# Kernel optimization log

Hardware: AMD Instinct MI355X
Metric: run time of the kernel (lower is better)

## Reference

```python
import jax, jax.numpy as jnp
import numpy as np

WINDOWS = [2, 4, 6]
THR = 0.5


def conv1x1(x, w, b):
    # x: [N,C,H,W], w: [O,C], b: [O]
    return jnp.einsum('nchw,oc->nohw', x, w) + b[None, :, None, None]


def cpool(x):
    # channel max + mean -> [N,2,H,W]
    return jnp.stack([x.max(axis=1), x.mean(axis=1)], axis=1)


def mask_fusion(orin, feature, w1, b1, w2, b2):
    sim = jax.nn.sigmoid(jnp.sum(conv1x1(cpool(orin), w1, b1) * conv1x1(cpool(feature), w2, b2), axis=1, keepdims=True))
    mask = (sim > THR).astype(orin.dtype)
    return mask * feature + (1.0 - mask) * orin


def unfold(x, kh, kw, sh, sw, w):
    # torch F.unfold equivalent -> [N, C*kh*kw, w*w] (channel-major like torch)
    rows = jnp.arange(w)[:, None] * sh + jnp.arange(kh)[None, :]  # [w,kh]
    cols = jnp.arange(w)[:, None] * sw + jnp.arange(kw)[None, :]  # [w,kw]
    p = x[:, :, rows[:, :, None, None], cols[None, None, :, :]]  # [N,C,w,kh,w,kw]
    p = p.transpose(0, 1, 3, 5, 2, 4)  # [N,C,kh,kw,w,w]
    N, C = x.shape[:2]
    return p.reshape(N, C * kh * kw, w * w)


def fold(cols_, H, W, kh, kw, sh, sw, w):
    # torch F.fold equivalent (col2im with overlap-add)
    N, CK, P = cols_.shape
    C = CK // (kh * kw)
    p = cols_.reshape(N, C, kh, kw, w, w).transpose(0, 1, 4, 2, 5, 3).reshape(N, C, w * kh, w * kw)
    r = (jnp.arange(w)[:, None] * sh + jnp.arange(kh)[None, :]).reshape(-1)
    c = (jnp.arange(w)[:, None] * sw + jnp.arange(kw)[None, :]).reshape(-1)
    return jnp.zeros((N, C, H, W), cols_.dtype).at[:, :, r[:, None], c[None, :]].add(p)


def psa(u, wq, wk, wv):
    # u: [N,C,P,L]; scaled dot-product self-attention over L within each patch
    t = u.transpose(0, 2, 3, 1)  # [N,P,L,C]
    q, k, v = t @ wq, t @ wk, t @ wv
    s = jnp.einsum('nplc,npmc->nplm', q, k) / jnp.sqrt(jnp.asarray(t.shape[-1], t.dtype))
    o = jnp.einsum('nplm,npmc->nplc', jax.nn.softmax(s, axis=-1), v)
    return o.transpose(0, 3, 1, 2)


def setup_inputs():
    key = jax.random.key(0)
    ks = jax.random.split(key, 20)
    N, C, H, W = 4, 64, 72, 72
    E = len(WINDOWS) * C
    nrm = lambda k, shape, s: jax.random.normal(k, shape, jnp.float32) * s
    return {
        'x': nrm(ks[0], (N, C, H, W), 1.0),
        'exp_w': nrm(ks[1], (E, C), C ** -0.5), 'exp_b': jnp.zeros((E,), jnp.float32),
        'res_w': nrm(ks[2], (C, E), E ** -0.5), 'res_b': jnp.zeros((C,), jnp.float32),
        'fus_w': nrm(ks[3], (C, C), C ** -0.5), 'fus_b': jnp.zeros((C,), jnp.float32),
        'wq': nrm(ks[4], (C, C), C ** -0.5),
        'wk': nrm(ks[5], (C, C), C ** -0.5),
        'wv': nrm(ks[6], (C, C), C ** -0.5),
        'mf1a_w': nrm(ks[7], (2, 2), 0.7), 'mf1a_b': jnp.zeros((2,), jnp.float32),
        'mf1b_w': nrm(ks[8], (2, 2), 0.7), 'mf1b_b': jnp.zeros((2,), jnp.float32),
        'mf2a_w': nrm(ks[9], (2, 2), 0.7), 'mf2a_b': jnp.zeros((2,), jnp.float32),
        'mf2b_w': nrm(ks[10], (2, 2), 0.7), 'mf2b_b': jnp.zeros((2,), jnp.float32),
    }


def reference(x, exp_w, exp_b, res_w, res_b, fus_w, fus_b, wq, wk, wv,
              mf1a_w, mf1a_b, mf1b_w, mf1b_b, mf2a_w, mf2a_b, mf2b_w, mf2b_b):
    N, C, H, W = x.shape
    expx = conv1x1(x, exp_w, exp_b)  # [N, 3C, H, W]
    parts = jnp.split(expx, len(WINDOWS), axis=1)
    outs = []
    for i, w in enumerate(WINDOWS):
        sh, sw = H // w, W // w
        kh, kw = sh + H % w, sw + W % w
        u = unfold(parts[i], kh, kw, sh, sw, w)       # [N, C*kh*kw, w*w]
        u = u.reshape(N, C, w * w, kh * kw)           # raw reinterpret, as in torch .view
        a = psa(u, wq, wk, wv).reshape(N, C * kh * kw, w * w)
        cnt = fold(jnp.ones_like(a), H, W, kh, kw, sh, sw, w)
        outs.append(fold(a, H, W, kh, kw, sh, sw, w) / cnt)
    out = mask_fusion(jnp.concatenate(outs, axis=1), expx, mf1a_w, mf1a_b, mf1b_w, mf1b_b)
    out = conv1x1(out, res_w, res_b)
    out = mask_fusion(out, x, mf2a_w, mf2a_b, mf2b_w, mf2b_b)
    return conv1x1(out, fus_w, fus_b)
```

## Files before the change

kernel.cpp:

```cpp
#include <hip/hip_runtime.h>

constexpr int CN = 4;
constexpr int CC = 64;
constexpr int CH = 72, CW = 72;
constexpr int HW = CH * CW;
constexpr int NPOS = CN * HW;
constexpr long TOKF = 3L * NPOS * 64;
constexpr long HPAD = 4096;

typedef _Float16 h4 __attribute__((ext_vector_type(4)));
typedef _Float16 h8 __attribute__((ext_vector_type(8)));
typedef float f4 __attribute__((ext_vector_type(4)));

__device__ __forceinline__ int fidx(int row, int g, int off) {
  return (row << 6) + ((g ^ (row & 7)) << 3) + off;
}
__device__ __forceinline__ int f192(int row, int g) {
  return row * 192 + (((g & 24) | ((g ^ row) & 7)) << 3);
}

template <int WW, int SS>
__device__ __forceinline__ void expand_body(const float* __restrict__ x,
                                            const float* __restrict__ w64,
                                            const float* __restrict__ b64,
                                            float* __restrict__ out, int pg) {
  int n = pg / HW;
  int pos = pg - n * HW;
  int h = pos / CW, wcol = pos % CW;

  float xv[64];
  const float* xp = x + (long)n * CC * HW + pos;
#pragma unroll
  for (int c = 0; c < 64; ++c) xv[c] = xp[c * HW];

  int wr = h / SS, kx = h % SS, wcq = wcol / SS, ky = wcol % SS;
  int j = kx * (SS * WW * WW) + ky * (WW * WW) + wr * WW + wcq;
  float* op = out + ((long)n * HW + j) * 64;

#pragma unroll 1
  for (int og = 0; og < 16; ++og) {
    float t0[4];
#pragma unroll
    for (int i = 0; i < 4; ++i) {
      int o = og * 4 + i;
      float acc = b64[o];
      const float* wp = w64 + o * 64;
#pragma unroll
      for (int cg = 0; cg < 16; ++cg) {
        float4 w4 = *(const float4*)(wp + 4 * cg);
        acc = fmaf(xv[4 * cg + 0], w4.x, acc);
        acc = fmaf(xv[4 * cg + 1], w4.y, acc);
        acc = fmaf(xv[4 * cg + 2], w4.z, acc);
        acc = fmaf(xv[4 * cg + 3], w4.w, acc);
      }
      t0[i] = acc;
    }
    *(float4*)(op + og * 4) = make_float4(t0[0], t0[1], t0[2], t0[3]);
  }
}

__global__ __launch_bounds__(256) void k_prep(
    const float* __restrict__ x, const float* __restrict__ exp_w,
    const float* __restrict__ exp_b, const float* __restrict__ wq,
    const float* __restrict__ wk, const float* __restrict__ wv,
    const float* __restrict__ res_w, const float* __restrict__ fus_w,
    float* __restrict__ ex, _Float16* __restrict__ wTh,
    _Float16* __restrict__ wTl, _Float16* __restrict__ rwh,
    _Float16* __restrict__ rwl, _Float16* __restrict__ fwh,
    _Float16* __restrict__ fwl) {
  int b = blockIdx.x;
  if (b >= 243) {
    int i = (b - 243) * 256 + threadIdx.x;
    float v;
    _Float16 *dh, *dl;
    int off;
    if (i < 12288) {
      int m = i >> 12;
      int r = i & 4095;
      int cp = r >> 6, c = r & 63;
      const float* src = (m == 0) ? wq : ((m == 1) ? wk : wv);
      v = src[c * 64 + cp];
      dh = wTh; dl = wTl; off = i;
    } else if (i < 24576) {
      off = i - 12288;
      v = res_w[off];
      dh = rwh; dl = rwl;
    } else {
      off = i - 24576;
      v = fus_w[off];
      dh = fwh; dl = fwl;
    }
    _Float16 h = (_Float16)v;
    dh[off] = h;
    dl[off] = (_Float16)(v - (float)h);
    return;
  }
  int wi = b / 81;
  int pg = (b - wi * 81) * 256 + threadIdx.x;
  if (wi == 0)
    expand_body<2, 36>(x, exp_w, exp_b, ex, pg);
  else if (wi == 1)
    expand_body<4, 18>(x, exp_w + 4096, exp_b + 64, ex + (long)NPOS * 64, pg);
  else
    expand_body<6, 12>(x, exp_w + 8192, exp_b + 128, ex + 2L * NPOS * 64, pg);
}

__global__ __launch_bounds__(256) void k_qkv(
    const float* __restrict__ ex, const _Float16* __restrict__ wTh,
    const _Float16* __restrict__ wTl, _Float16* __restrict__ qh,
    _Float16* __restrict__ ql, _Float16* __restrict__ kh,
    _Float16* __restrict__ kl, _Float16* __restrict__ vth,
    _Float16* __restrict__ vtl) {
  __shared__ __align__(16) _Float16 Wh[12288], Wl[12288];
  __shared__ __align__(16) float Cb[4096];
  _Float16* Eh = (_Float16*)Cb;
  _Float16* El = (_Float16*)Cb + 4096;

  const int tid = threadIdx.x;
  const long tok0 = (long)blockIdx.x * 64;
  const int lane = tid & 63, w = tid >> 6;
  const int lw = lane & 15, lg = lane >> 4;

  {
    int srow = tid >> 2, sfq = tid & 3;
#pragma unroll
    for (int p = 0; p < 4; ++p) {
      int c0 = (4 * p + sfq) * 4;
      float4 v = *(const float4*)(ex + (tok0 + srow) * 64 + c0);
      h4 hh = {(_Float16)v.x, (_Float16)v.y, (_Float16)v.z, (_Float16)v.w};
      h4 ll = {(_Float16)(v.x - (float)hh[0]), (_Float16)(v.y - (float)hh[1]),
               (_Float16)(v.z - (float)hh[2]), (_Float16)(v.w - (float)hh[3])};
      *(h4*)&Eh[fidx(srow, c0 >> 3, c0 & 7)] = hh;
      *(h4*)&El[fidx(srow, c0 >> 3, c0 & 7)] = ll;
    }
  }
#pragma unroll
  for (int it = 0; it < 6; ++it) {
    int idx = it * 256 + tid;
    int row = idx >> 3, gr = idx & 7;
    *(h8*)&Wh[fidx(row, gr, 0)] = *(const h8*)(wTh + idx * 8);
    *(h8*)&Wl[fidx(row, gr, 0)] = *(const h8*)(wTl + idx * 8);
  }
  __syncthreads();

  h8 eh[2], el[2];
#pragma unroll
  for (int s = 0; s < 2; ++s) {
    eh[s] = *(const h8*)&Eh[fidx(w * 16 + lw, s * 4 + lg, 0)];
    el[s] = *(const h8*)&El[fidx(w * 16 + lw, s * 4 + lg, 0)];
  }
  __syncthreads();

  const float SC = 0.125f * 1.4426950408889634f;
#pragma unroll 1
  for (int p = 0; p < 3; ++p) {
#pragma unroll
    for (int ot = 0; ot < 4; ++ot) {
      f4 acc = (f4){0.f, 0.f, 0.f, 0.f};
#pragma unroll
      for (int s = 0; s < 2; ++s) {
        h8 bh = *(const h8*)&Wh[fidx(p * 64 + ot * 16 + lw, s * 4 + lg, 0)];
        h8 bl = *(const h8*)&Wl[fidx(p * 64 + ot * 16 + lw, s * 4 + lg, 0)];
        acc = __builtin_amdgcn_mfma_f32_16x16x32_f16(eh[s], bh, acc, 0, 0, 0);
        acc = __builtin_amdgcn_mfma_f32_16x16x32_f16(el[s], bh, acc, 0, 0, 0);
        acc = __builtin_amdgcn_mfma_f32_16x16x32_f16(eh[s], bl, acc, 0, 0, 0);
      }
#pragma unroll
      for (int r = 0; r < 4; ++r) {
        int row = w * 16 + 4 * lg + r;
        int col = ot * 16 + lw;
        Cb[(row << 6) + ((((col >> 2) ^ (row & 15))) << 2) + (col & 3)] =
            acc[r];
      }
    }
    __syncthreads();

    if (p < 2) {
      int tokl = tid >> 2, off = (tid & 3) * 16;
      float vals[16];
#pragma unroll
      for (int j = 0; j < 4; ++j) {
        int slot = (off >> 2) + j;
        f4 v = *(const f4*)&Cb[(tokl << 6) + (((slot ^ (tokl & 15))) << 2)];
        vals[4 * j + 0] = v[0]; vals[4 * j + 1] = v[1];
        vals[4 * j + 2] = v[2]; vals[4 * j + 3] = v[3];
      }
      float sc = (p == 0) ? SC : 1.0f;
      _Float16* dh = (p == 0 ? qh : kh) + (tok0 + tokl) * 64 + off;
      _Float16* dl = (p == 0 ? ql : kl) + (tok0 + tokl) * 64 + off;
      h8 hh0, hh1, ll0, ll1;
#pragma unroll
      for (int j = 0; j < 8; ++j) {
        float x0 = vals[j] * sc;
        _Float16 h = (_Float16)x0;
        hh0[j] = h;
        ll0[j] = (_Float16)(x0 - (float)h);
        float x1 = vals[8 + j] * sc;
        _Float16 h1 = (_Float16)x1;
        hh1[j] = h1;
        ll1[j] = (_Float16)(x1 - (float)h1);
      }
      *(h8*)dh = hh0; *(h8*)(dh + 8) = hh1;
      *(h8*)dl = ll0; *(h8*)(dl + 8) = ll1;
    } else {
      int ch0 = (tid & 15) * 4, tokl0 = (tid >> 4) * 4;
      float tv[4][4];
#pragma unroll
      for (int r = 0; r < 4; ++r) {
        int row = tokl0 + r;
        int slot = (ch0 >> 2) ^ (row & 15);
        f4 v = *(const f4*)&Cb[(row << 6) + (slot << 2)];
        tv[r][0] = v[0]; tv[r][1] = v[1]; tv[r][2] = v[2]; tv[r][3] = v[3];
      }
      long tokg = tok0 + tokl0;
      int wi = (int)(tokg / NPOS);
      long tl = tokg - (long)wi * NPOS;
      int L = (wi == 0) ? 1296 : ((wi == 1) ? 324 : 144);
      int g = (int)(tl / L);
      int key0 = (int)(tl - (long)g * L);
      long base = (long)wi * NPOS * 64 + (long)g * 64 * L + key0;
#pragma unroll
      for (int i = 0; i < 4; ++i) {
        h4 hh, ll;
#pragma unroll
        for (int r = 0; r < 4; ++r) {
          _Float16 h = (_Float16)tv[r][i];
          hh[r] = h;
          ll[r] = (_Float16)(tv[r][i] - (float)h);
        }
        *(h4*)&vth[base + (long)(ch0 + i) * L] = hh;
        *(h4*)&vtl[base + (long)(ch0 + i) * L] = ll;
      }
    }
    __syncthreads();
  }
}

__global__ __launch_bounds__(256) void k_attn(
    const _Float16* __restrict__ qg, const _Float16* __restrict__ qgl,
    const _Float16* __restrict__ kg, const _Float16* __restrict__ kgl,
    const _Float16* __restrict__ vg, const _Float16* __restrict__ vgl,
    float* __restrict__ og_) {
  __shared__ __align__(16) _Float16 Kh[4096], Kl[4096];
  __shared__ __align__(16) _Float16 Vh[4096], Vl[4096];
  __shared__ __align__(16) _Float16 Ph[4096], Pl[4096];

  const int tid = threadIdx.x;
  int b = blockIdx.x;
  int L, g, qt, NCH;
  long tokbase, vbase;
  if (b < 336) {
    L = 1296; NCH = 21; g = b & 15; qt = b >> 4;
    tokbase = (long)g * 1296;
    vbase = (long)g * 1296 * 64;
  } else if (b < 720) {
    int t = b - 336;
    L = 324; NCH = 6; g = t & 63; qt = t >> 6;
    tokbase = (long)NPOS + (long)g * 324;
    vbase = (long)NPOS * 64 + (long)g * 324 * 64;
  } else {
    int t = b - 720;
    L = 144; NCH = 3; g = t % 144; qt = t / 144;
    tokbase = 2L * NPOS + (long)g * 144;
    vbase = 2L * NPOS * 64 + (long)g * 144 * 64;
  }

  const int lane = tid & 63, w = tid >> 6;
  const int lw = lane & 15, lg = lane >> 4;
  const int w16 = w * 16;

  h8 qfh[2], qfl[2];
  {
    long qb = (tokbase + (long)qt * 64 + w16 + lw) * 64;
#pragma unroll
    for (int s = 0; s < 2; ++s) {
      qfh[s] = *(const h8*)(qg + qb + (s * 4 + lg) * 8);
      qfl[s] = *(const h8*)(qgl + qb + (s * 4 + lg) * 8);
    }
  }

  float m_s = -1e30f, l_s = 0.f;
  f4 oa[4];
#pragma unroll
  for (int i = 0; i < 4; ++i) oa[i] = (f4){0.f, 0.f, 0.f, 0.f};

  const int krow = tid >> 3, kgr = tid & 7;
  const long ksA = (tokbase + krow) * 64 + kgr * 8;
  const long vsA = vbase + (long)krow * L + kgr * 8;
  const long v32 = (long)32 * L;

  h8 rk0, rk1, rl0, rl1, rv0, rv1, rw0, rw1;
  auto loadKV = [&](int chn) {
    long ko = ksA + ((long)chn << 12);
    long vo = vsA + chn * 64;
    rk0 = *(const h8*)(kg + ko);
    rl0 = *(const h8*)(kgl + ko);
    rv0 = *(const h8*)(vg + vo);
    rw0 = *(const h8*)(vgl + vo);
    rk1 = *(const h8*)(kg + ko + 2048);
    rl1 = *(const h8*)(kgl + ko + 2048);
    rv1 = *(const h8*)(vg + vo + v32);
    rw1 = *(const h8*)(vgl + vo + v32);
  };
  loadKV(0);

  for (int ch = 0; ch < NCH; ++ch) {
    __syncthreads();
    {
      *(h8*)&Kh[fidx(krow, kgr, 0)] = rk0;
      *(h8*)&Kl[fidx(krow, kgr, 0)] = rl0;
      *(h8*)&Vh[fidx(krow, kgr, 0)] = rv0;
      *(h8*)&Vl[fidx(krow, kgr, 0)] = rw0;
      *(h8*)&Kh[fidx(32 + krow, kgr, 0)] = rk1;
      *(h8*)&Kl[fidx(32 + krow, kgr, 0)] = rl1;
      *(h8*)&Vh[fidx(32 + krow, kgr, 0)] = rv1;
      *(h8*)&Vl[fidx(32 + krow, kgr, 0)] = rw1;
    }
    __syncthreads();
    if (ch + 1 < NCH) loadKV(ch + 1);

    f4 sa[4];
#pragma unroll
    for (int kt = 0; kt < 4; ++kt) sa[kt] = (f4){0.f, 0.f, 0.f, 0.f};
#pragma unroll
    for (int slab = 0; slab < 2; ++slab) {
      h8 qbh = qfh[slab];
      h8 qbl = qfl[slab];
#pragma unroll
      for (int kt = 0; kt < 4; ++kt) {
        h8 ah = *(const h8*)&Kh[fidx(kt * 16 + lw, slab * 4 + lg, 0)];
        h8 al = *(const h8*)&Kl[fidx(kt * 16 + lw, slab * 4 + lg, 0)];
        sa[kt] = __builtin_amdgcn_mfma_f32_16x16x32_f16(ah, qbh, sa[kt], 0, 0, 0);
        sa[kt] = __builtin_amdgcn_mfma_f32_16x16x32_f16(al, qbh, sa[kt], 0, 0, 0);
        sa[kt] = __builtin_amdgcn_mfma_f32_16x16x32_f16(ah, qbl, sa[kt], 0, 0, 0);
      }
    }

    float pr[4][4];
    float pmax = -1e30f;
#pragma unroll
    for (int kt = 0; kt < 4; ++kt)
#pragma unroll
      for (int r = 0; r < 4; ++r) {
        int kidx = ch * 64 + kt * 16 + 4 * lg + r;
        float s = (kidx < L) ? sa[kt][r] : -1e30f;
        pr[kt][r] = s;
        pmax = fmaxf(pmax, s);
      }
    pmax = fmaxf(pmax, __shfl_xor(pmax, 16));
    pmax = fmaxf(pmax, __shfl_xor(pmax, 32));
    if (!__all(pmax <= m_s + 8.0f)) {
      float mn = fmaxf(m_s, pmax);
      float fs = exp2f(m_s - mn);
      m_s = mn;
      float fsb[4];
#pragma unroll
      for (int r = 0; r < 4; ++r) fsb[r] = __shfl(fs, 4 * lg + r);
#pragma unroll
      for (int ct = 0; ct < 4; ++ct)
#pragma unroll
        for (int r = 0; r < 4; ++r) oa[ct][r] *= fsb[r];
      l_s *= fs;
    }
    float rs = 0.f;
#pragma unroll
    for (int kt = 0; kt < 4; ++kt)
#pragma unroll
      for (int r = 0; r < 4; ++r) {
        float e = exp2f(pr[kt][r] - m_s);
        pr[kt][r] = e;
        rs += e;
      }
    rs += __shfl_xor(rs, 16);
    rs += __shfl_xor(rs, 32);
    l_s += rs;

#pragma unroll
    for (int kt = 0; kt < 4; ++kt) {
      h4 hh = {(_Float16)pr[kt][0], (_Float16)pr[kt][1], (_Float16)pr[kt][2],
               (_Float16)pr[kt][3]};
      h4 ll = {(_Float16)(pr[kt][0] - (float)hh[0]),
               (_Float16)(pr[kt][1] - (float)hh[1]),
               (_Float16)(pr[kt][2] - (float)hh[2]),
               (_Float16)(pr[kt][3] - (float)hh[3])};
      int key0 = kt * 16 + 4 * lg;
      int kgr2 = key0 >> 3, ko = key0 & 7;
      *(h4*)&Ph[fidx(w16 + lw, kgr2, ko)] = hh;
      *(h4*)&Pl[fidx(w16 + lw, kgr2, ko)] = ll;
    }

#pragma unroll
    for (int slab = 0; slab < 2; ++slab) {
      h8 pah = *(const h8*)&Ph[fidx(w16 + lw, slab * 4 + lg, 0)];
      h8 pal = *(const h8*)&Pl[fidx(w16 + lw, slab * 4 + lg, 0)];
#pragma unroll
      for (int ct = 0; ct < 4; ++ct) {
        h8 vbh = *(const h8*)&Vh[fidx(ct * 16 + lw, slab * 4 + lg, 0)];
        h8 vbl = *(const h8*)&Vl[fidx(ct * 16 + lw, slab * 4 + lg, 0)];
        oa[ct] = __builtin_amdgcn_mfma_f32_16x16x32_f16(pah, vbh, oa[ct], 0, 0, 0);
        oa[ct] = __builtin_amdgcn_mfma_f32_16x16x32_f16(pal, vbh, oa[ct], 0, 0, 0);
        oa[ct] = __builtin_amdgcn_mfma_f32_16x16x32_f16(pah, vbl, oa[ct], 0, 0, 0);
      }
    }
  }

  float linv[4];
#pragma unroll
  for (int r = 0; r < 4; ++r) linv[r] = 1.0f / __shfl(l_s, 4 * lg + r);
#pragma unroll
  for (int r = 0; r < 4; ++r) {
    int qi = qt * 64 + w16 + 4 * lg + r;
    if (qi < L) {
      float* op = og_ + (tokbase + qi) * 64 + lw;
#pragma unroll
      for (int ct = 0; ct < 4; ++ct) op[ct * 16] = oa[ct][r] * linv[r];
    }
  }
}

__global__ __launch_bounds__(256) void k_fuse3(
    const float* __restrict__ x, const float* __restrict__ ex,
    const float* __restrict__ att, const float* __restrict__ m1aw,
    const float* __restrict__ m1ab, const float* __restrict__ m1bw,
    const float* __restrict__ m1bb, const _Float16* __restrict__ rwh,
    const _Float16* __restrict__ rwl, const float* __restrict__ res_b,
    const _Float16* __restrict__ fwh, const _Float16* __restrict__ fwl,
    const float* __restrict__ fus_b, const float* __restrict__ m2aw,
    const float* __restrict__ m2ab, const float* __restrict__ m2bw,
    const float* __restrict__ m2bb, float* __restrict__ out) {
  __shared__ __align__(16) _Float16 F1hS[12288];
  __shared__ __align__(16) _Float16 F1lS[12288];
  float* Cb = (float*)F1hS;
  _Float16* o2h = F1lS;
  _Float16* o2l = F1lS + 4096;

  const int tid = threadIdx.x;
  const int posb = blockIdx.x * 64;
  const int n = posb / HW, posn = posb % HW;
  const int lane = tid & 63, w = tid >> 6;
  const int lw = lane & 15, lg = lane >> 4;
  const int w16 = w * 16;

  {
    float w1a0 = m1aw[0], w1a1 = m1aw[1], w1a2 = m1aw[2], w1a3 = m1aw[3];
    float b1a0 = m1ab[0], b1a1 = m1ab[1];
    float w1b0 = m1bw[0], w1b1 = m1bw[1], w1b2 = m1bw[2], w1b3 = m1bw[3];
    float b1b0 = m1bb[0], b1b1 = m1bb[1];
#pragma unroll 1
    for (int pp = 0; pp < 16; ++pp) {
      int pl = w * 16 + pp;
      int pos = posn + pl;
      int h = pos / CW, wcol = pos % CW;
      auto tok = [&](int S, int W) -> int {
        int wr = h / S, kx = h % S, wcq = wcol / S, ky = wcol % S;
        return kx * (S * W * W) + ky * (W * W) + wr * W + wcq;
      };
      int j0 = tok(36, 2), j1 = tok(18, 4), j2 = tok(12, 6);
      long t0 = ((long)n * HW + j0) * 64 + lane;
      long t1 = ((long)NPOS + (long)n * HW + j1) * 64 + lane;
      long t2 = (2L * NPOS + (long)n * HW + j2) * 64 + lane;
      float av0 = att[t0], av1 = att[t1], av2 = att[t2];
      float ev0 = ex[t0], ev1 = ex[t1], ev2 = ex[t2];
      float mxa = fmaxf(fmaxf(av0, av1), av2), sma = av0 + av1 + av2;
      float mxe = fmaxf(fmaxf(ev0, ev1), ev2), sme = ev0 + ev1 + ev2;
#pragma unroll
      for (int d = 1; d < 64; d <<= 1) {
        mxa = fmaxf(mxa, __shfl_xor(mxa, d));
        sma += __shfl_xor(sma, d);
        mxe = fmaxf(mxe, __shfl_xor(mxe, d));
        sme += __shfl_xor(sme, d);
      }
      float mna = sma * (1.f / 192.f), mne = sme * (1.f / 192.f);
      float ca0 = fmaf(w1a0, mxa, fmaf(w1a1, mna, b1a0));
      float ca1 = fmaf(w1a2, mxa, fmaf(w1a3, mna, b1a1));
      float cb0 = fmaf(w1b0, mxe, fmaf(w1b1, mne, b1b0));
      float cb1 = fmaf(w1b2, mxe, fmaf(w1b3, mne, b1b1));
      bool mk = (ca0 * cb0 + ca1 * cb1) > 0.f;
      float v0 = mk ? ev0 : av0;
      float v1 = mk ? ev1 : av1;
      float v2 = mk ? ev2 : av2;
      _Float16 h0 = (_Float16)v0, h1 = (_Float16)v1, h2 = (_Float16)v2;
      int c0 = lane, c1 = lane + 64, c2 = lane + 128;
      F1hS[f192(pl, c0 >> 3) + (c0 & 7)] = h0;
      F1lS[f192(pl, c0 >> 3) + (c0 & 7)] = (_Float16)(v0 - (float)h0);
      F1hS[f192(pl, c1 >> 3) + (c1 & 7)] = h1;
      F1lS[f192(pl, c1 >> 3) + (c1 & 7)] = (_Float16)(v1 - (float)h1);
      F1hS[f192(pl, c2 >> 3) + (c2 & 7)] = h2;
      F1lS[f192(pl, c2 >> 3) + (c2 & 7)] = (_Float16)(v2 - (float)h2);
    }
  }
  __syncthreads();

  h8 ah[6], al[6];
#pragma unroll
  for (int s = 0; s < 6; ++s) {
    ah[s] = *(const h8*)&F1hS[f192(w16 + lw, s * 4 + lg)];
    al[s] = *(const h8*)&F1lS[f192(w16 + lw, s * 4 + lg)];
  }

  f4 acc[4];
#pragma unroll
  for (int ot = 0; ot < 4; ++ot) {
    float bb = res_b[ot * 16 + lw];
    acc[ot] = (f4){bb, bb, bb, bb};
#pragma unroll
    for (int s = 0; s < 6; ++s) {
      int wo = (ot * 16 + lw) * 192 + (s * 4 + lg) * 8;
      h8 bh = *(const h8*)(rwh + wo);
      h8 bl = *(const h8*)(rwl + wo);
      acc[ot] = __builtin_amdgcn_mfma_f32_16x16x32_f16(ah[s], bh, acc[ot], 0, 0, 0);
      acc[ot] = __builtin_amdgcn_mfma_f32_16x16x32_f16(al[s], bh, acc[ot], 0, 0, 0);
      acc[ot] = __builtin_amdgcn_mfma_f32_16x16x32_f16(ah[s], bl, acc[ot], 0, 0, 0);
    }
  }
  __syncthreads();

#pragma unroll
  for (int ot = 0; ot < 4; ++ot)
#pragma unroll
    for (int r = 0; r < 4; ++r) {
      int row = w16 + 4 * lg + r, col = ot * 16 + lw;
      Cb[(row << 6) + ((((col >> 2) ^ (row & 15))) << 2) + (col & 3)] =
          acc[ot][r];
    }
  __syncthreads();

  const int pos = tid >> 2, off = (tid & 3) * 16;
  float vals[16];
#pragma unroll
  for (int j = 0; j < 4; ++j) {
    int slot = (off >> 2) + j;
    f4 v = *(const f4*)&Cb[(pos << 6) + (((slot ^ (pos & 15))) << 2)];
    vals[4 * j + 0] = v[0]; vals[4 * j + 1] = v[1];
    vals[4 * j + 2] = v[2]; vals[4 * j + 3] = v[3];
  }
  float amx = vals[0], asum = vals[0];
#pragma unroll
  for (int i = 1; i < 16; ++i) {
    amx = fmaxf(amx, vals[i]);
    asum += vals[i];
  }
  amx = fmaxf(amx, __shfl_xor(amx, 1)); asum += __shfl_xor(asum, 1);
  amx = fmaxf(amx, __shfl_xor(amx, 2)); asum += __shfl_xor(asum, 2);
  float xv[16];
  const float* xp = x + ((long)n * CC + off) * HW + posn + pos;
#pragma unroll
  for (int i = 0; i < 16; ++i) xv[i] = xp[i * HW];
  float xmx = xv[0], xsum = xv[0];
#pragma unroll
  for (int i = 1; i < 16; ++i) {
    xmx = fmaxf(xmx, xv[i]);
    xsum += xv[i];
  }
  xmx = fmaxf(xmx, __shfl_xor(xmx, 1)); xsum += __shfl_xor(xsum, 1);
  xmx = fmaxf(xmx, __shfl_xor(xmx, 2)); xsum += __shfl_xor(xsum, 2);
  float rmn = asum * (1.f / 64.f), xmn = xsum * (1.f / 64.f);
  float ca0 = fmaf(m2aw[0], amx, fmaf(m2aw[1], rmn, m2ab[0]));
  float ca1 = fmaf(m2aw[2], amx, fmaf(m2aw[3], rmn, m2ab[1]));
  float cb0 = fmaf(m2bw[0], xmx, fmaf(m2bw[1], xmn, m2bb[0]));
  float cb1 = fmaf(m2bw[2], xmx, fmaf(m2bw[3], xmn, m2bb[1]));
  bool mk2 = (ca0 * cb0 + ca1 * cb1) > 0.f;

#pragma unroll
  for (int hf = 0; hf < 2; ++hf) {
    h8 hh, ll;
#pragma unroll
    for (int j = 0; j < 8; ++j) {
      float v = mk2 ? xv[hf * 8 + j] : vals[hf * 8 + j];
      _Float16 hx = (_Float16)v;
      hh[j] = hx;
      ll[j] = (_Float16)(v - (float)hx);
    }
    int g = (off >> 3) + hf;
    *(h8*)&o2h[fidx(pos, g, 0)] = hh;
    *(h8*)&o2l[fidx(pos, g, 0)] = ll;
  }
  __syncthreads();

  h8 a2h[2], a2l[2];
#pragma unroll
  for (int s = 0; s < 2; ++s) {
    a2h[s] = *(const h8*)&o2h[fidx(w16 + lw, s * 4 + lg, 0)];
    a2l[s] = *(const h8*)&o2l[fidx(w16 + lw, s * 4 + lg, 0)];
  }
  f4 acc2[4];
#pragma unroll
  for (int ot = 0; ot < 4; ++ot) {
    float bb = fus_b[ot * 16 + lw];
    acc2[ot] = (f4){bb, bb, bb, bb};
#pragma unroll
    for (int s = 0; s < 2; ++s) {
      int wo = (ot * 16 + lw) * 64 + (s * 4 + lg) * 8;
      h8 bh = *(const h8*)(fwh + wo);
      h8 bl = *(const h8*)(fwl + wo);
      acc2[ot] = __builtin_amdgcn_mfma_f32_16x16x32_f16(a2h[s], bh, acc2[ot], 0, 0, 0);
      acc2[ot] = __builtin_amdgcn_mfma_f32_16x16x32_f16(a2l[s], bh, acc2[ot], 0, 0, 0);
      acc2[ot] = __builtin_amdgcn_mfma_f32_16x16x32_f16(a2h[s], bl, acc2[ot], 0, 0, 0);
    }
  }
  __syncthreads();

#pragma unroll
  for (int ot = 0; ot < 4; ++ot)
#pragma unroll
    for (int r = 0; r < 4; ++r) {
      int prow = w16 + 4 * lg + r, col = ot * 16 + lw;
      Cb[(prow << 6) + ((col + prow) & 63)] = acc2[ot][r];
    }
  __syncthreads();
#pragma unroll
  for (int i = 0; i < 16; ++i) {
    float v = Cb[(lane << 6) + ((w16 + i + lane) & 63)];
    out[((long)n * CC + w16 + i) * HW + posn + lane] = v;
  }
}

extern "C" void kernel_launch(void* const* d_in, const int* in_sizes, int n_in,
                              void* d_out, int out_size, void* d_ws,
                              size_t ws_size, hipStream_t stream) {
  (void)in_sizes; (void)n_in; (void)out_size;
  const float* x      = (const float*)d_in[0];
  const float* exp_w  = (const float*)d_in[1];
  const float* exp_b  = (const float*)d_in[2];
  const float* res_w  = (const float*)d_in[3];
  const float* res_b  = (const float*)d_in[4];
  const float* fus_w  = (const float*)d_in[5];
  const float* fus_b  = (const float*)d_in[6];
  const float* wq     = (const float*)d_in[7];
  const float* wk     = (const float*)d_in[8];
  const float* wv     = (const float*)d_in[9];
  const float* m1aw   = (const float*)d_in[10];
  const float* m1ab   = (const float*)d_in[11];
  const float* m1bw   = (const float*)d_in[12];
  const float* m1bb   = (const float*)d_in[13];
  const float* m2aw   = (const float*)d_in[14];
  const float* m2ab   = (const float*)d_in[15];
  const float* m2bw   = (const float*)d_in[16];
  const float* m2bb   = (const float*)d_in[17];

  const long HSZ = TOKF + HPAD;
  const size_t needF =
      2 * (size_t)TOKF + (6 * (size_t)HSZ + 2 * 12288 + 2 * 12288 + 2 * 4096) / 2;
  if (ws_size < needF * sizeof(float)) return;
  float* ws = (float*)d_ws;
  float* ex = ws;
  float* ob = ex + TOKF;
  _Float16* qh  = (_Float16*)(ob + TOKF);
  _Float16* ql  = qh + HSZ;
  _Float16* kh  = ql + HSZ;
  _Float16* kl  = kh + HSZ;
  _Float16* vth = kl + HSZ;
  _Float16* vtl = vth + HSZ;
  _Float16* wTh = vtl + HSZ;
  _Float16* wTl = wTh + 12288;
  _Float16* rwh = wTl + 12288;
  _Float16* rwl = rwh + 12288;
  _Float16* fwh = rwl + 12288;
  _Float16* fwl = fwh + 4096;

  k_prep<<<355, 256, 0, stream>>>(x, exp_w, exp_b, wq, wk, wv, res_w, fus_w,
                                  ex, wTh, wTl, rwh, rwl, fwh, fwl);
  k_qkv<<<972, 256, 0, stream>>>(ex, wTh, wTl, qh, ql, kh, kl, vth, vtl);
  k_attn<<<1152, 256, 0, stream>>>(qh, ql, kh, kl, vth, vtl, ob);
  k_fuse3<<<324, 256, 0, stream>>>(x, ex, ob, m1aw, m1ab, m1bw, m1bb, rwh,
                                   rwl, res_b, fwh, fwl, fus_b, m2aw, m2ab,
                                   m2bw, m2bb, (float*)d_out);
}
```

Baseline: 153.1 us.

## Process two 16-query fragments per wave in attention with 128-thread blocks

The attention kernel now uses 2 waves per block instead of 4. Each wave handles 32 query rows as two 16-row fragments, so every K and V fragment read from LDS feeds two sets of MFMAs, which halves LDS read traffic per MFMA. Cooperative K/V staging now has 128 threads each loading four rows. The cost is roughly double the accumulator and Q-fragment registers, which may lower occupancy, and fewer waves are available per block to hide latency.

```diff
diff --git a/kernel.cpp b/kernel.cpp
--- a/kernel.cpp
+++ b/kernel.cpp
@@ -236,7 +236,7 @@
   }
 }
 
-__global__ __launch_bounds__(256) void k_attn(
+__global__ __launch_bounds__(128) void k_attn(
     const _Float16* __restrict__ qg, const _Float16* __restrict__ qgl,
     const _Float16* __restrict__ kg, const _Float16* __restrict__ kgl,
     const _Float16* __restrict__ vg, const _Float16* __restrict__ vgl,
@@ -265,155 +265,179 @@
     vbase = 2L * NPOS * 64 + (long)g * 144 * 64;
   }
 
-  const int lane = tid & 63, w = tid >> 6;
+  const int lane = tid & 63, wq = tid >> 6;
   const int lw = lane & 15, lg = lane >> 4;
-  const int w16 = w * 16;
-
-  h8 qfh[2], qfl[2];
-  {
-    long qb = (tokbase + (long)qt * 64 + w16 + lw) * 64;
+  const int qw = wq * 32;
+
+  h8 qfh[2][2], qfl[2][2];
+#pragma unroll
+  for (int qf = 0; qf < 2; ++qf) {
+    long qb = (tokbase + (long)qt * 64 + qw + 16 * qf + lw) * 64;
 #pragma unroll
     for (int s = 0; s < 2; ++s) {
-      qfh[s] = *(const h8*)(qg + qb + (s * 4 + lg) * 8);
-      qfl[s] = *(const h8*)(qgl + qb + (s * 4 + lg) * 8);
-    }
-  }
-
-  float m_s = -1e30f, l_s = 0.f;
-  f4 oa[4];
-#pragma unroll
-  for (int i = 0; i < 4; ++i) oa[i] = (f4){0.f, 0.f, 0.f, 0.f};
-
-  const int krow = tid >> 3, kgr = tid & 7;
-  const long ksA = (tokbase + krow) * 64 + kgr * 8;
-  const long vsA = vbase + (long)krow * L + kgr * 8;
-  const long v32 = (long)32 * L;
-
-  h8 rk0, rk1, rl0, rl1, rv0, rv1, rw0, rw1;
+      qfh[qf][s] = *(const h8*)(qg + qb + (s * 4 + lg) * 8);
+      qfl[qf][s] = *(const h8*)(qgl + qb + (s * 4 + lg) * 8);
+    }
+  }
+
+  float m_s[2] = {-1e30f, -1e30f}, l_s[2] = {0.f, 0.f};
+  f4 oa[2][4];
+#pragma unroll
+  for (int qf = 0; qf < 2; ++qf)
+#pragma unroll
+    for (int i = 0; i < 4; ++i) oa[qf][i] = (f4){0.f, 0.f, 0.f, 0.f};
+
+  const int srow = tid >> 3, kgr = tid & 7;
+  const long ksA = (tokbase + srow) * 64 + kgr * 8;
+  const long vsA = vbase + (long)srow * L + kgr * 8;
+  const long v16 = (long)16 * L;
+
+  h8 rk[4], rl[4], rv[4], rw[4];
   auto loadKV = [&](int chn) {
     long ko = ksA + ((long)chn << 12);
     long vo = vsA + chn * 64;
-    rk0 = *(const h8*)(kg + ko);
-    rl0 = *(const h8*)(kgl + ko);
-    rv0 = *(const h8*)(vg + vo);
-    rw0 = *(const h8*)(vgl + vo);
-    rk1 = *(const h8*)(kg + ko + 2048);
-    rl1 = *(const h8*)(kgl + ko + 2048);
-    rv1 = *(const h8*)(vg + vo + v32);
-    rw1 = *(const h8*)(vgl + vo + v32);
+#pragma unroll
+    for (int r = 0; r < 4; ++r) {
+      rk[r] = *(const h8*)(kg + ko + r * 1024);
+      rl[r] = *(const h8*)(kgl + ko + r * 1024);
+      rv[r] = *(const h8*)(vg + vo + r * v16);
+      rw[r] = *(const h8*)(vgl + vo + r * v16);
+    }
   };
   loadKV(0);
 
   for (int ch = 0; ch < NCH; ++ch) {
     __syncthreads();
-    {
-      *(h8*)&Kh[fidx(krow, kgr, 0)] = rk0;
-      *(h8*)&Kl[fidx(krow, kgr, 0)] = rl0;
-      *(h8*)&Vh[fidx(krow, kgr, 0)] = rv0;
-      *(h8*)&Vl[fidx(krow, kgr, 0)] = rw0;
-      *(h8*)&Kh[fidx(32 + krow, kgr, 0)] = rk1;
-      *(h8*)&Kl[fidx(32 + krow, kgr, 0)] = rl1;
-      *(h8*)&Vh[fidx(32 + krow, kgr, 0)] = rv1;
-      *(h8*)&Vl[fidx(32 + krow, kgr, 0)] = rw1;
+#pragma unroll
+    for (int r = 0; r < 4; ++r) {
+      int row = r * 16 + srow;
+      *(h8*)&Kh[fidx(row, kgr, 0)] = rk[r];
+      *(h8*)&Kl[fidx(row, kgr, 0)] = rl[r];
+      *(h8*)&Vh[fidx(row, kgr, 0)] = rv[r];
+      *(h8*)&Vl[fidx(row, kgr, 0)] = rw[r];
     }
     __syncthreads();
     if (ch + 1 < NCH) loadKV(ch + 1);
 
-    f4 sa[4];
-#pragma unroll
-    for (int kt = 0; kt < 4; ++kt) sa[kt] = (f4){0.f, 0.f, 0.f, 0.f};
+    f4 sa[2][4];
+#pragma unroll
+    for (int qf = 0; qf < 2; ++qf)
+#pragma unroll
+      for (int kt = 0; kt < 4; ++kt) sa[qf][kt] = (f4){0.f, 0.f, 0.f, 0.f};
 #pragma unroll
     for (int slab = 0; slab < 2; ++slab) {
-      h8 qbh = qfh[slab];
-      h8 qbl = qfl[slab];
 #pragma unroll
       for (int kt = 0; kt < 4; ++kt) {
         h8 ah = *(const h8*)&Kh[fidx(kt * 16 + lw, slab * 4 + lg, 0)];
         h8 al = *(const h8*)&Kl[fidx(kt * 16 + lw, slab * 4 + lg, 0)];
-        sa[kt] = __builtin_amdgcn_mfma_f32_16x16x32_f16(ah, qbh, sa[kt], 0, 0, 0);
-        sa[kt] = __builtin_amdgcn_mfma_f32_16x16x32_f16(al, qbh, sa[kt], 0, 0, 0);
-        sa[kt] = __builtin_amdgcn_mfma_f32_16x16x32_f16(ah, qbl, sa[kt], 0, 0, 0);
-      }
-    }
-
-    float pr[4][4];
-    float pmax = -1e30f;
-#pragma unroll
-    for (int kt = 0; kt < 4; ++kt)
-#pragma unroll
-      for (int r = 0; r < 4; ++r) {
-        int kidx = ch * 64 + kt * 16 + 4 * lg + r;
-        float s = (kidx < L) ? sa[kt][r] : -1e30f;
-        pr[kt][r] = s;
-        pmax = fmaxf(pmax, s);
-      }
-    pmax = fmaxf(pmax, __shfl_xor(pmax, 16));
-    pmax = fmaxf(pmax, __shfl_xor(pmax, 32));
-    if (!__all(pmax <= m_s + 8.0f)) {
-      float mn = fmaxf(m_s, pmax);
-      float fs = exp2f(m_s - mn);
-      m_s = mn;
-      float fsb[4];
-#pragma unroll
-      for (int r = 0; r < 4; ++r) fsb[r] = __shfl(fs, 4 * lg + r);
-#pragma unroll
-      for (int ct = 0; ct < 4; ++ct)
-#pragma unroll
-        for (int r = 0; r < 4; ++r) oa[ct][r] *= fsb[r];
-      l_s *= fs;
-    }
-    float rs = 0.f;
-#pragma unroll
-    for (int kt = 0; kt < 4; ++kt)
-#pragma unroll
-      for (int r = 0; r < 4; ++r) {
-        float e = exp2f(pr[kt][r] - m_s);
-        pr[kt][r] = e;
-        rs += e;
-      }
-    rs += __shfl_xor(rs, 16);
-    rs += __shfl_xor(rs, 32);
-    l_s += rs;
-
-#pragma unroll
-    for (int kt = 0; kt < 4; ++kt) {
-      h4 hh = {(_Float16)pr[kt][0], (_Float16)pr[kt][1], (_Float16)pr[kt][2],
-               (_Float16)pr[kt][3]};
-      h4 ll = {(_Float16)(pr[kt][0] - (float)hh[0]),
-               (_Float16)(pr[kt][1] - (float)hh[1]),
-               (_Float16)(pr[kt][2] - (float)hh[2]),
-               (_Float16)(pr[kt][3] - (float)hh[3])};
-      int key0 = kt * 16 + 4 * lg;
-      int kgr2 = key0 >> 3, ko = key0 & 7;
-      *(h4*)&Ph[fidx(w16 + lw, kgr2, ko)] = hh;
-      *(h4*)&Pl[fidx(w16 + lw, kgr2, ko)] = ll;
+#pragma unroll
+        for (int qf = 0; qf < 2; ++qf) {
+          sa[qf][kt] = __builtin_amdgcn_mfma_f32_16x16x32_f16(
+              ah, qfh[qf][slab], sa[qf][kt], 0, 0, 0);
+          sa[qf][kt] = __builtin_amdgcn_mfma_f32_16x16x32_f16(
+              al, qfh[qf][slab], sa[qf][kt], 0, 0, 0);
+          sa[qf][kt] = __builtin_amdgcn_mfma_f32_16x16x32_f16(
+              ah, qfl[qf][slab], sa[qf][kt], 0, 0, 0);
+        }
+      }
+    }
+
+#pragma unroll
+    for (int qf = 0; qf < 2; ++qf) {
+      float pr[4][4];
+      float pmax = -1e30f;
+#pragma unroll
+      for (int kt = 0; kt < 4; ++kt)
+#pragma unroll
+        for (int r = 0; r < 4; ++r) {
+          int kidx = ch * 64 + kt * 16 + 4 * lg + r;
+          float s = (kidx < L) ? sa[qf][kt][r] : -1e30f;
+          pr[kt][r] = s;
+          pmax = fmaxf(pmax, s);
+        }
+      pmax = fmaxf(pmax, __shfl_xor(pmax, 16));
+      pmax = fmaxf(pmax, __shfl_xor(pmax, 32));
+      if (!__all(pmax <= m_s[qf] + 8.0f)) {
+        float mn = fmaxf(m_s[qf], pmax);
+        float fs = exp2f(m_s[qf] - mn);
+        m_s[qf] = mn;
+        float fsb[4];
+#pragma unroll
+        for (int r = 0; r < 4; ++r) fsb[r] = __shfl(fs, 4 * lg + r);
+#pragma unroll
+        for (int ct = 0; ct < 4; ++ct)
+#pragma unroll
+          for (int r = 0; r < 4; ++r) oa[qf][ct][r] *= fsb[r];
+        l_s[qf] *= fs;
+      }
+      float rs = 0.f;
+#pragma unroll
+      for (int kt = 0; kt < 4; ++kt)
+#pragma unroll
+        for (int r = 0; r < 4; ++r) {
+          float e = exp2f(pr[kt][r] - m_s[qf]);
+          pr[kt][r] = e;
+          rs += e;
+        }
+      rs += __shfl_xor(rs, 16);
+      rs += __shfl_xor(rs, 32);
+      l_s[qf] += rs;
+
+#pragma unroll
+      for (int kt = 0; kt < 4; ++kt) {
+        h4 hh = {(_Float16)pr[kt][0], (_Float16)pr[kt][1],
+                 (_Float16)pr[kt][2], (_Float16)pr[kt][3]};
+        h4 ll = {(_Float16)(pr[kt][0] - (float)hh[0]),
+                 (_Float16)(pr[kt][1] - (float)hh[1]),
+                 (_Float16)(pr[kt][2] - (float)hh[2]),
+                 (_Float16)(pr[kt][3] - (float)hh[3])};
+        int key0 = kt * 16 + 4 * lg;
+        int kgr2 = key0 >> 3, ko = key0 & 7;
+        int prow = qw + 16 * qf + lw;
+        *(h4*)&Ph[fidx(prow, kgr2, ko)] = hh;
+        *(h4*)&Pl[fidx(prow, kgr2, ko)] = ll;
+      }
     }
 
 #pragma unroll
     for (int slab = 0; slab < 2; ++slab) {
-      h8 pah = *(const h8*)&Ph[fidx(w16 + lw, slab * 4 + lg, 0)];
-      h8 pal = *(const h8*)&Pl[fidx(w16 + lw, slab * 4 + lg, 0)];
+      h8 pah[2], pal[2];
+#pragma unroll
+      for (int qf = 0; qf < 2; ++qf) {
+        int prow = qw + 16 * qf + lw;
+        pah[qf] = *(const h8*)&Ph[fidx(prow, slab * 4 + lg, 0)];
+        pal[qf] = *(const h8*)&Pl[fidx(prow, slab * 4 + lg, 0)];
+      }
 #pragma unroll
       for (int ct = 0; ct < 4; ++ct) {
         h8 vbh = *(const h8*)&Vh[fidx(ct * 16 + lw, slab * 4 + lg, 0)];
         h8 vbl = *(const h8*)&Vl[fidx(ct * 16 + lw, slab * 4 + lg, 0)];
-        oa[ct] = __builtin_amdgcn_mfma_f32_16x16x32_f16(pah, vbh, oa[ct], 0, 0, 0);
-        oa[ct] = __builtin_amdgcn_mfma_f32_16x16x32_f16(pal, vbh, oa[ct], 0, 0, 0);
-        oa[ct] = __builtin_amdgcn_mfma_f32_16x16x32_f16(pah, vbl, oa[ct], 0, 0, 0);
-      }
-    }
-  }
-
-  float linv[4];
-#pragma unroll
-  for (int r = 0; r < 4; ++r) linv[r] = 1.0f / __shfl(l_s, 4 * lg + r);
-#pragma unroll
-  for (int r = 0; r < 4; ++r) {
-    int qi = qt * 64 + w16 + 4 * lg + r;
-    if (qi < L) {
-      float* op = og_ + (tokbase + qi) * 64 + lw;
-#pragma unroll
-      for (int ct = 0; ct < 4; ++ct) op[ct * 16] = oa[ct][r] * linv[r];
+#pragma unroll
+        for (int qf = 0; qf < 2; ++qf) {
+          oa[qf][ct] = __builtin_amdgcn_mfma_f32_16x16x32_f16(
+              pah[qf], vbh, oa[qf][ct], 0, 0, 0);
+          oa[qf][ct] = __builtin_amdgcn_mfma_f32_16x16x32_f16(
+              pal[qf], vbh, oa[qf][ct], 0, 0, 0);
+          oa[qf][ct] = __builtin_amdgcn_mfma_f32_16x16x32_f16(
+              pah[qf], vbl, oa[qf][ct], 0, 0, 0);
+        }
+      }
+    }
+  }
+
+#pragma unroll
+  for (int qf = 0; qf < 2; ++qf) {
+    float linv[4];
+#pragma unroll
+    for (int r = 0; r < 4; ++r) linv[r] = 1.0f / __shfl(l_s[qf], 4 * lg + r);
+#pragma unroll
+    for (int r = 0; r < 4; ++r) {
+      int qi = qt * 64 + qw + 16 * qf + 4 * lg + r;
+      if (qi < L) {
+        float* op = og_ + (tokbase + qi) * 64 + lw;
+#pragma unroll
+        for (int ct = 0; ct < 4; ++ct) op[ct * 16] = oa[qf][ct][r] * linv[r];
+      }
     }
   }
 }
@@ -661,7 +685,7 @@
   k_prep<<<355, 256, 0, stream>>>(x, exp_w, exp_b, wq, wk, wv, res_w, fus_w,
                                   ex, wTh, wTl, rwh, rwl, fwh, fwl);
   k_qkv<<<972, 256, 0, stream>>>(ex, wTh, wTl, qh, ql, kh, kl, vth, vtl);
-  k_attn<<<1152, 256, 0, stream>>>(qh, ql, kh, kl, vth, vtl, ob);
+  k_attn<<<1152, 128, 0, stream>>>(qh, ql, kh, kl, vth, vtl, ob);
   k_fuse3<<<324, 256, 0, stream>>>(x, ex, ob, m1aw, m1ab, m1bw, m1bb, rwh,
                                    rwl, res_b, fwh, fwl, fus_b, m2aw, m2ab,
                                    m2bw, m2bb, (float*)d_out);
```

Measured after the change: 169.9 us. 11.0% more time.
